# Performance work log

Measured on AMD Instinct MI355X. Metric: run time of the kernel, lower is better.

Reference implementation:

```python
import jax, jax.numpy as jnp
import numpy as np

B, C, T, L = 32, 256, 4096, 1024  # lines, codec classes, frames, tokens per line (T >= 2L)


def setup_inputs() -> dict:
    key = jax.random.key(0)
    k1, k2 = jax.random.split(key)
    logits = jax.random.normal(k1, (B, C, T), dtype=jnp.float32)
    # token labels are codec indices; 0 is the CTC blank, so draw from [1, C)
    tokens = jax.random.randint(k2, (B, L), 1, C, dtype=jnp.int32)
    return {"logits": logits, "tokens": tokens}


def _trellis(emission, tokens):
    # emission: [T, C] log-probs, tokens: [L] -> trellis [T+1, L+1]
    Tn = emission.shape[0]
    Ln = tokens.shape[0]
    col0 = jnp.concatenate([jnp.zeros((1,), emission.dtype),
                            jnp.cumsum(emission[:, 0])])
    col0 = col0.at[-Ln:].set(jnp.inf)          # trellis[-L:, 0] = +inf
    row0 = jnp.concatenate([jnp.zeros((1,), emission.dtype),
                            jnp.full((Ln,), -jnp.inf, emission.dtype)])  # trellis[0]

    def step(prev, inp):
        e_t, c0_next = inp                      # e_t: [C], c0_next: scalar col0[t+1]
        stay = prev[1:] + e_t[0]                # stay on same token (blank emission)
        change = prev[:-1] + e_t[tokens]        # advance to next token
        new = jnp.concatenate([c0_next[None], jnp.maximum(stay, change)])
        return new, new

    _, rows = jax.lax.scan(step, row0, (emission, col0[1:]))
    return jnp.concatenate([row0[None], rows], axis=0)  # [T+1, L+1]


def _backtrack(trellis, emission, tokens):
    # Fixed-length (T steps) masked backtrack; emits path in reverse time order.
    Tn = emission.shape[0]
    Ln = tokens.shape[0]
    t_start = jnp.argmax(trellis[:, -1]).astype(jnp.int32)

    def step(carry, k):
        j, done = carry
        t = t_start - k
        active = (t >= 1) & jnp.logical_not(done)
        tm1 = jnp.maximum(t - 1, 0)
        jm1 = jnp.maximum(j - 1, 0)
        stayed = trellis[tm1, j] + emission[tm1, 0]
        changed = trellis[tm1, jm1] + emission[tm1, tokens[jm1]]
        take = changed > stayed
        prob = jnp.exp(jnp.where(take, emission[tm1, tokens[jm1]], emission[tm1, 0]))
        out = (jm1, tm1, prob, active)
        j_new = jnp.where(active & take, j - 1, j)
        done_new = done | (j_new == 0) | (t <= 1)
        return (j_new, done_new), out

    init = (jnp.int32(Ln), jnp.array(False))
    _, (pj, pt, pp, pv) = jax.lax.scan(step, init, jnp.arange(Tn, dtype=jnp.int32))
    return pj, pt, pp, pv


def reference(logits, tokens):
    # emission = logits.squeeze().log_softmax(0).T, batched: [B, T, C]
    emission = jax.nn.log_softmax(logits, axis=1).transpose(0, 2, 1)
    trellis = jax.vmap(_trellis)(emission, tokens)              # [B, T+1, L+1]
    pj, pt, pp, pv = jax.vmap(_backtrack)(trellis, emission, tokens)
    return trellis, pj, pt, pp, pv
```

## Files before the change

kernel.cpp:

```cpp
#include <hip/hip_runtime.h>
#include <math.h>

#define B_ 32
#define C_ 256
#define T_ 4096
#define L_ 1024

__device__ __forceinline__ float clamp_store(float x) {
  return fminf(fmaxf(x, -1e30f), 1e30f);
}

#define DB_OFF   ((size_t)524416)
#define JOUT_OFF ((size_t)17301632)
#define WS_NEED  ((size_t)17563776)

__global__ __launch_bounds__(256) void lse_kernel(const float* __restrict__ logits,
                                                  float* __restrict__ lse) {
  const int b  = blockIdx.x >> 8;
  const int t0 = (blockIdx.x & 255) << 4;
  const int c  = threadIdx.x;
  const float* p = logits + (((size_t)b << 8) + (size_t)c) * T_ + t0;
  float4 v0 = *(const float4*)(p + 0);
  float4 v1 = *(const float4*)(p + 4);
  float4 v2 = *(const float4*)(p + 8);
  float4 v3 = *(const float4*)(p + 12);

  __shared__ float lds[16][257];
  lds[ 0][c] = v0.x; lds[ 1][c] = v0.y; lds[ 2][c] = v0.z; lds[ 3][c] = v0.w;
  lds[ 4][c] = v1.x; lds[ 5][c] = v1.y; lds[ 6][c] = v1.z; lds[ 7][c] = v1.w;
  lds[ 8][c] = v2.x; lds[ 9][c] = v2.y; lds[10][c] = v2.z; lds[11][c] = v2.w;
  lds[12][c] = v3.x; lds[13][c] = v3.y; lds[14][c] = v3.z; lds[15][c] = v3.w;
  __syncthreads();

  const int w = threadIdx.x >> 6, lane = threadIdx.x & 63;
  for (int s = w; s < 16; s += 4) {
    float x0 = lds[s][lane], x1 = lds[s][lane + 64];
    float x2 = lds[s][lane + 128], x3 = lds[s][lane + 192];
    float m = fmaxf(fmaxf(x0, x1), fmaxf(x2, x3));
#pragma unroll
    for (int d = 32; d; d >>= 1) m = fmaxf(m, __shfl_xor(m, d, 64));
    float sum = expf(x0 - m) + expf(x1 - m) + expf(x2 - m) + expf(x3 - m);
#pragma unroll
    for (int d = 32; d; d >>= 1) sum += __shfl_xor(sum, d, 64);
    if (lane == 0) lse[b * T_ + t0 + s] = m + logf(sum);
  }
}

__global__ __launch_bounds__(1024) void trellis_kernel(const float* __restrict__ logits,
                                                       const int* __restrict__ tokens,
                                                       const float* __restrict__ lseg,
                                                       float* __restrict__ out,
                                                       unsigned long long* __restrict__ db) {
  const int b = blockIdx.x;
  const int tid = threadIdx.x;
  const int lane = tid & 63, w = tid >> 6;

  __shared__ float se[C_ * 20];
  __shared__ float s_lse[16];
  __shared__ float s_bnd[2][16];

  const int tok = tokens[b * L_ + tid];
  float* tre = out + (size_t)b * (T_ + 1) * (L_ + 1);

  tre[tid + 1] = -1e30f;
  if (tid == 0) tre[0] = 0.f;

  float prev = -INFINITY;
  if (lane == 63) s_bnd[0][w] = prev;
  float cum = 0.f, c0 = 0.f;

  const int c = tid >> 2, q = tid & 3;
  const float* lbase = logits + ((size_t)b * C_ + (size_t)c) * T_;
  const float* lsep = lseg + b * T_;
  const bool wdb = (db != nullptr);
  unsigned long long* dbrow = wdb ? db + ((size_t)b * L_ + tid) * 64 : nullptr;
  unsigned long long dmask = 0ull;

  float4 stg = *(const float4*)(lbase + 4 * q);
  float lse_stg = (tid < 16) ? lsep[tid] : 0.f;

  for (int chunk = 0; chunk < T_ / 16; ++chunk) {
    const int t0 = chunk << 4;
    *(float4*)(se + c * 20 + 4 * q) = stg;
    if (tid < 16) s_lse[tid] = lse_stg;
    __syncthreads();

    if (chunk + 1 < T_ / 16) {
      stg = *(const float4*)(lbase + (t0 + 16) + 4 * q);
      if (tid < 16) lse_stg = lsep[t0 + 16 + tid];
    }

    float4 ea = *(const float4*)(se + tok * 20 + 0);
    float4 eb = *(const float4*)(se + tok * 20 + 4);
    float4 ec4 = *(const float4*)(se + tok * 20 + 8);
    float4 ed = *(const float4*)(se + tok * 20 + 12);
    float ev[16] = {ea.x, ea.y, ea.z, ea.w, eb.x, eb.y, eb.z, eb.w,
                    ec4.x, ec4.y, ec4.z, ec4.w, ed.x, ed.y, ed.z, ed.w};

#pragma unroll
    for (int s = 0; s < 16; ++s) {
      const int t = t0 + s;
      const float ls = s_lse[s];
      const float e0 = se[s] - ls;
      const float et = ev[s] - ls;
      float prevL = __shfl_up(prev, 1, 64);
      if (lane == 0) prevL = (w == 0) ? c0 : s_bnd[t & 1][w - 1];
      const float stay = prev + e0;
      const float chng = prevL + et;
      const float nv = fmaxf(stay, chng);
      dmask |= (unsigned long long)(chng > stay) << (((chunk & 3) << 4) | s);
      if (s == 15 && (chunk & 3) == 3) {
        if (wdb) dbrow[t >> 6] = dmask;
        dmask = 0ull;
      }
      cum += e0;
      const float c0n = (t + 1 >= T_ + 1 - L_) ? INFINITY : cum;
      float* row = tre + (size_t)(t + 1) * (L_ + 1);
      row[tid + 1] = clamp_store(nv);
      if (tid == 0) row[0] = clamp_store(c0n);
      if (lane == 63) s_bnd[(t + 1) & 1][w] = nv;
      prev = nv;
      c0 = c0n;
      __syncthreads();
    }
  }
}

__global__ __launch_bounds__(256) void argmax_kernel(const float* __restrict__ out,
                                                     int* __restrict__ tstart) {
  const int b = blockIdx.x;
  const float* tre = out + (size_t)b * (T_ + 1) * (L_ + 1);
  float bv = -INFINITY;
  int bi = 0x7fffffff;
  for (int t = threadIdx.x; t <= T_; t += 256) {
    float v = tre[(size_t)t * (L_ + 1) + L_];
    if (v > bv || (v == bv && t < bi)) { bv = v; bi = t; }
  }
  __shared__ float sv[256];
  __shared__ int si[256];
  sv[threadIdx.x] = bv; si[threadIdx.x] = bi;
  __syncthreads();
  for (int d = 128; d; d >>= 1) {
    if (threadIdx.x < d) {
      float ov = sv[threadIdx.x + d]; int oi = si[threadIdx.x + d];
      if (ov > sv[threadIdx.x] || (ov == sv[threadIdx.x] && oi < si[threadIdx.x])) {
        sv[threadIdx.x] = ov; si[threadIdx.x] = oi;
      }
    }
    __syncthreads();
  }
  if (threadIdx.x == 0) tstart[b] = si[0];
}

__global__ __launch_bounds__(64) void backtrack_path_kernel(
    const unsigned long long* __restrict__ db,
    const int* __restrict__ tstart,
    unsigned short* __restrict__ jout) {
  const int b = blockIdx.x;
  if (threadIdx.x != 0) return;
  const int ts = tstart[b];
  unsigned short* jo = jout + (size_t)b * T_;
  const unsigned long long* dbb = db + (size_t)b * L_ * 64;
  int j = L_;
  int k = 0;
  bool done = false;
  while (k < T_) {
    const int t = ts - k;
    if (done || t < 1) {
      const unsigned short v = (unsigned short)j;
      for (; k < T_; ++k) jo[k] = v;
      break;
    }
    const unsigned long long* row = dbb + (size_t)(j - 1) * 64;
    const int p = t - 1;
    int w = p >> 6;
    unsigned long long word = row[w] & (~0ull >> (63 - (p & 63)));
    int tTake = 0;
    while (true) {
      if (word) { tTake = (w << 6) + (63 - __clzll(word)) + 1; break; }
      if (--w < 0) break;
      word = row[w];
    }
    const unsigned short v = (unsigned short)(j | 0x8000);
    if (tTake >= 1) {
      const int kTake = ts - tTake;
      for (; k <= kTake; ++k) jo[k] = v;
      j -= 1;
      done = (j == 0) || (tTake <= 1);
    } else {
      const int kEnd = ts - 1;
      for (; k <= kEnd; ++k) jo[k] = v;
      done = true;
    }
  }
}

__global__ __launch_bounds__(256) void backtrack_emit_kernel(
    const float* __restrict__ logits, const int* __restrict__ tokens,
    const float* __restrict__ lseg, const int* __restrict__ tstart,
    const unsigned short* __restrict__ jout, float* __restrict__ out) {
  const int idx = blockIdx.x * 256 + threadIdx.x;
  const int b = idx >> 12;
  const int k = idx & (T_ - 1);
  const float* tre = out + (size_t)b * (T_ + 1) * (L_ + 1);
  const float* lg = logits + (size_t)b * C_ * T_;
  const int ts = tstart[b];
  const unsigned short pk = jout[(size_t)b * T_ + k];
  const int j = pk & 0x7fff;
  const bool active = (pk & 0x8000) != 0;
  const int t = ts - k;
  const int tm1 = (t - 1 > 0) ? t - 1 : 0;
  const int jm1 = (j - 1 > 0) ? j - 1 : 0;
  const float ls = lseg[b * T_ + tm1];
  const float e0 = lg[tm1] - ls;
  const int tk = tokens[b * L_ + jm1];
  const float ec = lg[(size_t)tk * T_ + tm1] - ls;
  const float stayed = tre[(size_t)tm1 * (L_ + 1) + j] + e0;
  const float changed = tre[(size_t)tm1 * (L_ + 1) + jm1] + ec;
  const bool take = changed > stayed;
  const size_t OBASE = (size_t)B_ * (T_ + 1) * (L_ + 1);
  float* pj = out + OBASE + (size_t)b * T_;
  float* pt = pj + (size_t)B_ * T_;
  float* pp = pt + (size_t)B_ * T_;
  float* pv = pp + (size_t)B_ * T_;
  pj[k] = (float)jm1;
  pt[k] = (float)tm1;
  pp[k] = expf(take ? ec : e0);
  pv[k] = active ? 1.f : 0.f;
}

__global__ __launch_bounds__(64) void backtrack_kernel(const float* __restrict__ logits,
                                                       const int* __restrict__ tokens,
                                                       const float* __restrict__ lseg,
                                                       const int* __restrict__ tstart,
                                                       float* __restrict__ out) {
  const int b = blockIdx.x;
  if (threadIdx.x != 0) return;
  const float* tre = out + (size_t)b * (T_ + 1) * (L_ + 1);
  const float* lg = logits + (size_t)b * C_ * T_;
  const float* lsep = lseg + b * T_;
  const int* tkp = tokens + b * L_;
  const size_t OBASE = (size_t)B_ * (T_ + 1) * (L_ + 1);
  float* pj = out + OBASE + (size_t)b * T_;
  float* pt = pj + (size_t)B_ * T_;
  float* pp = pt + (size_t)B_ * T_;
  float* pv = pp + (size_t)B_ * T_;

  const int ts = tstart[b];
  int j = L_;
  bool done = false;
  for (int k = 0; k < T_; ++k) {
    const int t = ts - k;
    const bool active = (t >= 1) && !done;
    const int tm1 = (t - 1 > 0) ? t - 1 : 0;
    const int jm1 = (j - 1 > 0) ? j - 1 : 0;
    const float ls = lsep[tm1];
    const float e0 = lg[tm1] - ls;
    const int tk = tkp[jm1];
    const float ec = lg[(size_t)tk * T_ + tm1] - ls;
    const float stayed = tre[(size_t)tm1 * (L_ + 1) + j] + e0;
    const float changed = tre[(size_t)tm1 * (L_ + 1) + jm1] + ec;
    const bool take = changed > stayed;
    pj[k] = (float)jm1;
    pt[k] = (float)tm1;
    pp[k] = expf(take ? ec : e0);
    pv[k] = active ? 1.f : 0.f;
    if (active && take) j -= 1;
    done = done || (j == 0) || (t <= 1);
  }
}

extern "C" void kernel_launch(void* const* d_in, const int* in_sizes, int n_in,
                              void* d_out, int out_size, void* d_ws, size_t ws_size,
                              hipStream_t stream) {
  const float* logits = (const float*)d_in[0];
  const int* tokens = (const int*)d_in[1];
  float* out = (float*)d_out;
  float* lse = (float*)d_ws;
  int* tstart = (int*)(lse + (size_t)B_ * T_);

  const bool fast = (ws_size >= WS_NEED);
  unsigned long long* db =
      fast ? (unsigned long long*)((char*)d_ws + DB_OFF) : nullptr;
  unsigned short* jout =
      fast ? (unsigned short*)((char*)d_ws + JOUT_OFF) : nullptr;

  lse_kernel<<<B_ * (T_ / 16), 256, 0, stream>>>(logits, lse);
  trellis_kernel<<<B_, 1024, 0, stream>>>(logits, tokens, lse, out, db);
  argmax_kernel<<<B_, 256, 0, stream>>>(out, tstart);
  if (fast) {
    backtrack_path_kernel<<<B_, 64, 0, stream>>>(db, tstart, jout);
    backtrack_emit_kernel<<<B_ * (T_ / 256), 256, 0, stream>>>(
        logits, tokens, lse, tstart, jout, out);
  } else {
    backtrack_kernel<<<B_, 64, 0, stream>>>(logits, tokens, lse, tstart, out);
  }
}
```

Before: 2.204 ms.

## Replace per-step block barriers with per-chunk halo recompute across waves

Removes the __syncthreads after every time step in the trellis recurrence. At the start of each 16-step chunk, each wave takes a snapshot of the previous wave's 64 columns and recomputes them locally in a rotated register copy. This gives it its left boundary for every step without waiting on another wave. Shared emission and lse buffers are double-buffered so one barrier per chunk is enough. In exchange, each wave does roughly twice the recurrence arithmetic and makes extra shared-memory loads for the halo tokens.

Measured after the change: 2.005 ms. 1.1x faster.

```diff
diff --git a/kernel.cpp b/kernel.cpp
--- a/kernel.cpp
+++ b/kernel.cpp
@@ -55,18 +55,19 @@
   const int tid = threadIdx.x;
   const int lane = tid & 63, w = tid >> 6;
 
-  __shared__ float se[C_ * 20];
-  __shared__ float s_lse[16];
-  __shared__ float s_bnd[2][16];
+  __shared__ float se[2][C_ * 20];
+  __shared__ float s_lse[2][16];
+  __shared__ float s_pub[2][16][64];
 
   const int tok = tokens[b * L_ + tid];
+  const int tokh = (w > 0) ? tokens[b * L_ + tid - 64] : 0;
   float* tre = out + (size_t)b * (T_ + 1) * (L_ + 1);
 
   tre[tid + 1] = -1e30f;
   if (tid == 0) tre[0] = 0.f;
 
-  float prev = -INFINITY;
-  if (lane == 63) s_bnd[0][w] = prev;
+  float v = -INFINITY;
+  float h = -INFINITY;
   float cum = 0.f, c0 = 0.f;
 
   const int c = tid >> 2, q = tid & 3;
@@ -76,39 +77,76 @@
   unsigned long long* dbrow = wdb ? db + ((size_t)b * L_ + tid) * 64 : nullptr;
   unsigned long long dmask = 0ull;
 
+  const int rotIdx = (lane + 63) & 63;
+
   float4 stg = *(const float4*)(lbase + 4 * q);
   float lse_stg = (tid < 16) ? lsep[tid] : 0.f;
 
   for (int chunk = 0; chunk < T_ / 16; ++chunk) {
+    const int par = chunk & 1;
     const int t0 = chunk << 4;
-    *(float4*)(se + c * 20 + 4 * q) = stg;
-    if (tid < 16) s_lse[tid] = lse_stg;
+    float* sp = &se[par][0];
+    *(float4*)(sp + c * 20 + 4 * q) = stg;
+    if (tid < 16) s_lse[par][tid] = lse_stg;
+    s_pub[par][w][lane] = v;
     __syncthreads();
 
     if (chunk + 1 < T_ / 16) {
       stg = *(const float4*)(lbase + (t0 + 16) + 4 * q);
       if (tid < 16) lse_stg = lsep[t0 + 16 + tid];
     }
-
-    float4 ea = *(const float4*)(se + tok * 20 + 0);
-    float4 eb = *(const float4*)(se + tok * 20 + 4);
-    float4 ec4 = *(const float4*)(se + tok * 20 + 8);
-    float4 ed = *(const float4*)(se + tok * 20 + 12);
-    float ev[16] = {ea.x, ea.y, ea.z, ea.w, eb.x, eb.y, eb.z, eb.w,
+    if (w > 0) h = s_pub[par][w - 1][lane];
+
+    const float4* lf = (const float4*)&s_lse[par][0];
+    float4 L0 = lf[0], L1 = lf[1], L2 = lf[2], L3 = lf[3];
+    float lsv[16] = {L0.x, L0.y, L0.z, L0.w, L1.x, L1.y, L1.z, L1.w,
+                     L2.x, L2.y, L2.z, L2.w, L3.x, L3.y, L3.z, L3.w};
+    float4 za = *(const float4*)(sp + 0);
+    float4 zb = *(const float4*)(sp + 4);
+    float4 zc = *(const float4*)(sp + 8);
+    float4 zd = *(const float4*)(sp + 12);
+    float r0[16] = {za.x, za.y, za.z, za.w, zb.x, zb.y, zb.z, zb.w,
+                    zc.x, zc.y, zc.z, zc.w, zd.x, zd.y, zd.z, zd.w};
+    float4 ea = *(const float4*)(sp + tok * 20 + 0);
+    float4 eb = *(const float4*)(sp + tok * 20 + 4);
+    float4 ec4 = *(const float4*)(sp + tok * 20 + 8);
+    float4 ed = *(const float4*)(sp + tok * 20 + 12);
+    float rt[16] = {ea.x, ea.y, ea.z, ea.w, eb.x, eb.y, eb.z, eb.w,
                     ec4.x, ec4.y, ec4.z, ec4.w, ed.x, ed.y, ed.z, ed.w};
+    float rh[16];
+    if (w > 0) {
+      float4 ha = *(const float4*)(sp + tokh * 20 + 0);
+      float4 hb = *(const float4*)(sp + tokh * 20 + 4);
+      float4 hc = *(const float4*)(sp + tokh * 20 + 8);
+      float4 hd = *(const float4*)(sp + tokh * 20 + 12);
+      rh[0] = ha.x; rh[1] = ha.y; rh[2] = ha.z; rh[3] = ha.w;
+      rh[4] = hb.x; rh[5] = hb.y; rh[6] = hb.z; rh[7] = hb.w;
+      rh[8] = hc.x; rh[9] = hc.y; rh[10] = hc.z; rh[11] = hc.w;
+      rh[12] = hd.x; rh[13] = hd.y; rh[14] = hd.z; rh[15] = hd.w;
+    } else {
+#pragma unroll
+      for (int s = 0; s < 16; ++s) rh[s] = 0.f;
+    }
+    float e0v[16], etv[16], eth[16];
+#pragma unroll
+    for (int s = 0; s < 16; ++s) {
+      e0v[s] = r0[s] - lsv[s];
+      etv[s] = rt[s] - lsv[s];
+      eth[s] = rh[s] - lsv[s];
+    }
 
 #pragma unroll
     for (int s = 0; s < 16; ++s) {
       const int t = t0 + s;
-      const float ls = s_lse[s];
-      const float e0 = se[s] - ls;
-      const float et = ev[s] - ls;
-      float prevL = __shfl_up(prev, 1, 64);
-      if (lane == 0) prevL = (w == 0) ? c0 : s_bnd[t & 1][w - 1];
-      const float stay = prev + e0;
-      const float chng = prevL + et;
-      const float nv = fmaxf(stay, chng);
-      dmask |= (unsigned long long)(chng > stay) << (((chunk & 3) << 4) | s);
+      const float e0 = e0v[s];
+      const float hRot = __shfl(h, rotIdx, 64);
+      const float vUp = __shfl_up(v, 1, 64);
+      const float vL = (lane == 0) ? ((w == 0) ? c0 : hRot) : vUp;
+      h = fmaxf(h + e0, hRot + eth[s]);
+      const float stay = v + e0;
+      const float chg = vL + etv[s];
+      const float nv = fmaxf(stay, chg);
+      dmask |= (unsigned long long)(chg > stay) << (((chunk & 3) << 4) | s);
       if (s == 15 && (chunk & 3) == 3) {
         if (wdb) dbrow[t >> 6] = dmask;
         dmask = 0ull;
@@ -118,10 +156,8 @@
       float* row = tre + (size_t)(t + 1) * (L_ + 1);
       row[tid + 1] = clamp_store(nv);
       if (tid == 0) row[0] = clamp_store(c0n);
-      if (lane == 63) s_bnd[(t + 1) & 1][w] = nv;
-      prev = nv;
+      v = nv;
       c0 = c0n;
-      __syncthreads();
     }
   }
 }
```

## Run trellis DP in one wavefront per batch and parallelize backtrack path search

Applied to the files above, without the earlier changes.

The trellis kernel moves from a 1024-thread block that did a __syncthreads per time step to a single 64-lane wavefront in which each lane holds 16 consecutive trellis columns in registers. The cross-lane dependency is handled with a shuffle instead of block barriers. Emission values are now read straight from global memory at token offsets rather than staged through LDS. The backtrack path kernel uses all 64 lanes: a ballot over the 64 decision words finds the last take bit, the next rows are prefetched, and output fills run in parallel. The intent is to remove per-step block synchronization and serial backtrack scanning, at the cost of far fewer threads per batch and uncoalesced gathered loads.

Result: slower. 3.074 ms (+39.5%).

```diff
diff --git a/kernel.cpp b/kernel.cpp
--- a/kernel.cpp
+++ b/kernel.cpp
@@ -6,9 +6,6 @@
 #define T_ 4096
 #define L_ 1024
 
-__device__ __forceinline__ float clamp_store(float x) {
-  return fminf(fmaxf(x, -1e30f), 1e30f);
-}
 
 #define DB_OFF   ((size_t)524416)
 #define JOUT_OFF ((size_t)17301632)
@@ -46,82 +43,125 @@
   }
 }
 
-__global__ __launch_bounds__(1024) void trellis_kernel(const float* __restrict__ logits,
-                                                       const int* __restrict__ tokens,
-                                                       const float* __restrict__ lseg,
-                                                       float* __restrict__ out,
-                                                       unsigned long long* __restrict__ db) {
+__global__ __launch_bounds__(64) void trellis_kernel(const float* __restrict__ logits,
+                                                     const int* __restrict__ tokens,
+                                                     const float* __restrict__ lseg,
+                                                     float* __restrict__ out,
+                                                     unsigned long long* __restrict__ db) {
   const int b = blockIdx.x;
-  const int tid = threadIdx.x;
-  const int lane = tid & 63, w = tid >> 6;
-
-  __shared__ float se[C_ * 20];
-  __shared__ float s_lse[16];
-  __shared__ float s_bnd[2][16];
-
-  const int tok = tokens[b * L_ + tid];
+  const int lane = threadIdx.x;
+  const int j0 = lane << 4;
+  const bool lane0 = (lane == 0);
+
+  const float* lgb = logits + (size_t)b * C_ * T_;
+  const float* lg0 = lgb;
+  const float* lsp = lseg + b * T_;
   float* tre = out + (size_t)b * (T_ + 1) * (L_ + 1);
-
-  tre[tid + 1] = -1e30f;
-  if (tid == 0) tre[0] = 0.f;
-
-  float prev = -INFINITY;
-  if (lane == 63) s_bnd[0][w] = prev;
-  float cum = 0.f, c0 = 0.f;
-
-  const int c = tid >> 2, q = tid & 3;
-  const float* lbase = logits + ((size_t)b * C_ + (size_t)c) * T_;
-  const float* lsep = lseg + b * T_;
   const bool wdb = (db != nullptr);
-  unsigned long long* dbrow = wdb ? db + ((size_t)b * L_ + tid) * 64 : nullptr;
-  unsigned long long dmask = 0ull;
-
-  float4 stg = *(const float4*)(lbase + 4 * q);
-  float lse_stg = (tid < 16) ? lsep[tid] : 0.f;
-
-  for (int chunk = 0; chunk < T_ / 16; ++chunk) {
-    const int t0 = chunk << 4;
-    *(float4*)(se + c * 20 + 4 * q) = stg;
-    if (tid < 16) s_lse[tid] = lse_stg;
-    __syncthreads();
-
-    if (chunk + 1 < T_ / 16) {
-      stg = *(const float4*)(lbase + (t0 + 16) + 4 * q);
-      if (tid < 16) lse_stg = lsep[t0 + 16 + tid];
-    }
-
-    float4 ea = *(const float4*)(se + tok * 20 + 0);
-    float4 eb = *(const float4*)(se + tok * 20 + 4);
-    float4 ec4 = *(const float4*)(se + tok * 20 + 8);
-    float4 ed = *(const float4*)(se + tok * 20 + 12);
-    float ev[16] = {ea.x, ea.y, ea.z, ea.w, eb.x, eb.y, eb.z, eb.w,
-                    ec4.x, ec4.y, ec4.z, ec4.w, ed.x, ed.y, ed.z, ed.w};
-
-#pragma unroll
-    for (int s = 0; s < 16; ++s) {
-      const int t = t0 + s;
-      const float ls = s_lse[s];
-      const float e0 = se[s] - ls;
-      const float et = ev[s] - ls;
-      float prevL = __shfl_up(prev, 1, 64);
-      if (lane == 0) prevL = (w == 0) ? c0 : s_bnd[t & 1][w - 1];
-      const float stay = prev + e0;
-      const float chng = prevL + et;
-      const float nv = fmaxf(stay, chng);
-      dmask |= (unsigned long long)(chng > stay) << (((chunk & 3) << 4) | s);
-      if (s == 15 && (chunk & 3) == 3) {
-        if (wdb) dbrow[t >> 6] = dmask;
-        dmask = 0ull;
+  unsigned long long* dbl = db + (size_t)b * L_ * 64;
+
+  int off[17];
+#pragma unroll
+  for (int kk = 0; kk < 17; ++kk) {
+    int idx = j0 + kk - 1;
+    idx = idx < 0 ? 0 : idx;
+    off[kk] = tokens[b * L_ + idx] * T_;
+  }
+
+  float v[17];
+#pragma unroll
+  for (int kk = 0; kk < 17; ++kk) v[kk] = -1e30f;
+  if (lane0) v[0] = 0.f;
+  float cum = 0.f;
+
+  {
+    float4 o;
+    o.x = v[0]; o.y = v[1]; o.z = v[2]; o.w = v[3];
+    *(float4*)(tre + j0 + 0) = o;
+    o.x = v[4]; o.y = v[5]; o.z = v[6]; o.w = v[7];
+    *(float4*)(tre + j0 + 4) = o;
+    o.x = v[8]; o.y = v[9]; o.z = v[10]; o.w = v[11];
+    *(float4*)(tre + j0 + 8) = o;
+    o.x = v[12]; o.y = v[13]; o.z = v[14]; o.w = v[15];
+    *(float4*)(tre + j0 + 12) = o;
+    if (lane == 63) tre[L_] = v[16];
+  }
+
+  float* rowp = tre + (L_ + 1);
+  unsigned acc[16];
+#pragma unroll
+  for (int kk = 0; kk < 16; ++kk) acc[kk] = 0u;
+
+  auto run32 = [&](int tbase) {
+#pragma unroll 1
+    for (int c8 = 0; c8 < 8; ++c8) {
+      const int t0 = tbase + (c8 << 2);
+      float4 gk[17];
+#pragma unroll
+      for (int kk = 0; kk < 17; ++kk)
+        gk[kk] = *(const float4*)(lgb + (off[kk] + t0));
+      const float4 lsw = *(const float4*)(lsp + t0);
+      const float4 zw = *(const float4*)(lg0 + t0);
+#pragma unroll
+      for (int s = 0; s < 4; ++s) {
+        const int t = t0 + s;
+        const float lss = ((const float*)&lsw)[s];
+        const float em0 = ((const float*)&zw)[s] - lss;
+        const float bnd = __shfl_up(v[15], 1, 64);
+#pragma unroll
+        for (int kk = 16; kk >= 1; --kk) {
+          const float em = ((const float*)&gk[kk])[s] - lss;
+          const float stay = v[kk] + em0;
+          const float chg = v[kk - 1] + em;
+          v[kk] = fmaxf(stay, chg);
+          acc[kk - 1] = (acc[kk - 1] << 1) | (unsigned)(chg > stay);
+        }
+        {
+          const float em = ((const float*)&gk[0])[s] - lss;
+          const float stay = v[0] + em0;
+          const float chg = bnd + em;
+          const float nv0 = fmaxf(stay, chg);
+          cum += em0;
+          const float c0n = (t + 1 >= T_ + 1 - L_) ? 1e30f : cum;
+          v[0] = lane0 ? c0n : nv0;
+        }
+        float4 o;
+        o.x = v[0]; o.y = v[1]; o.z = v[2]; o.w = v[3];
+        *(float4*)(rowp + j0 + 0) = o;
+        o.x = v[4]; o.y = v[5]; o.z = v[6]; o.w = v[7];
+        *(float4*)(rowp + j0 + 4) = o;
+        o.x = v[8]; o.y = v[9]; o.z = v[10]; o.w = v[11];
+        *(float4*)(rowp + j0 + 8) = o;
+        o.x = v[12]; o.y = v[13]; o.z = v[14]; o.w = v[15];
+        *(float4*)(rowp + j0 + 12) = o;
+        if (lane == 63) rowp[L_] = v[16];
+        rowp += (L_ + 1);
       }
-      cum += e0;
-      const float c0n = (t + 1 >= T_ + 1 - L_) ? INFINITY : cum;
-      float* row = tre + (size_t)(t + 1) * (L_ + 1);
-      row[tid + 1] = clamp_store(nv);
-      if (tid == 0) row[0] = clamp_store(c0n);
-      if (lane == 63) s_bnd[(t + 1) & 1][w] = nv;
-      prev = nv;
-      c0 = c0n;
-      __syncthreads();
+    }
+  };
+
+#pragma unroll 1
+  for (int win = 0; win < 64; ++win) {
+    run32(win * 64);
+    unsigned wlo[16];
+#pragma unroll
+    for (int kk = 0; kk < 16; ++kk) {
+      wlo[kk] = __builtin_bitreverse32(acc[kk]);
+      acc[kk] = 0u;
+    }
+    run32(win * 64 + 32);
+    if (wdb) {
+#pragma unroll
+      for (int kk = 0; kk < 16; ++kk) {
+        const unsigned long long wd =
+            (unsigned long long)wlo[kk] |
+            ((unsigned long long)__builtin_bitreverse32(acc[kk]) << 32);
+        dbl[(size_t)(j0 + kk) * 64 + win] = wd;
+        acc[kk] = 0u;
+      }
+    } else {
+#pragma unroll
+      for (int kk = 0; kk < 16; ++kk) acc[kk] = 0u;
     }
   }
 }
@@ -157,41 +197,54 @@
     const int* __restrict__ tstart,
     unsigned short* __restrict__ jout) {
   const int b = blockIdx.x;
-  if (threadIdx.x != 0) return;
+  const int lane = threadIdx.x;
   const int ts = tstart[b];
   unsigned short* jo = jout + (size_t)b * T_;
   const unsigned long long* dbb = db + (size_t)b * L_ * 64;
+
+  auto fill = [&](int k0, int k1, int val) {
+    for (int kk = k0 + lane; kk <= k1; kk += 64) jo[kk] = (unsigned short)val;
+  };
+
+  if (ts < 1) {
+    fill(0, T_ - 1, L_);
+    return;
+  }
+
   int j = L_;
-  int k = 0;
-  bool done = false;
-  while (k < T_) {
-    const int t = ts - k;
-    if (done || t < 1) {
-      const unsigned short v = (unsigned short)j;
-      for (; k < T_; ++k) jo[k] = v;
-      break;
-    }
-    const unsigned long long* row = dbb + (size_t)(j - 1) * 64;
+  int t = ts;
+  auto rowload = [&](int r) {
+    r = r < 0 ? 0 : r;
+    return dbb[(size_t)r * 64 + lane];
+  };
+  unsigned long long r0 = rowload(j - 1), r1 = rowload(j - 2),
+                     r2 = rowload(j - 3), r3 = rowload(j - 4);
+
+  while (true) {
     const int p = t - 1;
-    int w = p >> 6;
-    unsigned long long word = row[w] & (~0ull >> (63 - (p & 63)));
-    int tTake = 0;
-    while (true) {
-      if (word) { tTake = (w << 6) + (63 - __clzll(word)) + 1; break; }
-      if (--w < 0) break;
-      word = row[w];
-    }
-    const unsigned short v = (unsigned short)(j | 0x8000);
-    if (tTake >= 1) {
-      const int kTake = ts - tTake;
-      for (; k <= kTake; ++k) jo[k] = v;
-      j -= 1;
-      done = (j == 0) || (tTake <= 1);
-    } else {
-      const int kEnd = ts - 1;
-      for (; k <= kEnd; ++k) jo[k] = v;
-      done = true;
-    }
+    const int wcur = p >> 6;
+    unsigned long long w = r0;
+    if (lane > wcur) w = 0ull;
+    else if (lane == wcur) w &= (~0ull >> (63 - (p & 63)));
+    const unsigned long long nz = __ballot(w != 0ull);
+    if (nz == 0ull) {
+      fill(ts - t, ts - 1, j | 0x8000);
+      fill(ts, T_ - 1, j);
+      return;
+    }
+    const int hl = 63 - __clzll(nz);
+    const unsigned long long wh = __shfl(w, hl, 64);
+    const int tTake = (hl << 6) + (63 - __clzll(wh)) + 1;
+    const int kTake = ts - tTake;
+    fill(ts - t, kTake, j | 0x8000);
+    j -= 1;
+    if (j == 0 || tTake <= 1) {
+      fill(kTake + 1, T_ - 1, j);
+      return;
+    }
+    t = tTake - 1;
+    r0 = r1; r1 = r2; r2 = r3;
+    r3 = rowload(j - 4);
   }
 }
 
@@ -286,7 +339,7 @@
       fast ? (unsigned short*)((char*)d_ws + JOUT_OFF) : nullptr;
 
   lse_kernel<<<B_ * (T_ / 16), 256, 0, stream>>>(logits, lse);
-  trellis_kernel<<<B_, 1024, 0, stream>>>(logits, tokens, lse, out, db);
+  trellis_kernel<<<B_, 64, 0, stream>>>(logits, tokens, lse, out, db);
   argmax_kernel<<<B_, 256, 0, stream>>>(out, tstart);
   if (fast) {
     backtrack_path_kernel<<<B_, 64, 0, stream>>>(db, tstart, jout);
```
